# Kernel tuning notes

Hardware: AMD Instinct MI355X
Metric: run time of the kernel (lower is better)

Reference implementation:

```python
import jax, jax.numpy as jnp
import numpy as np

N = 8192
D_IN = 128
D_OUT = 128

def setup_inputs() -> dict:
    key = jax.random.key(0)
    k_x, k_q, k_k, k_v = jax.random.split(key, 4)
    scale = 1.0 / np.sqrt(D_IN)
    return {
        "input": jax.random.normal(k_x, (N, D_IN), dtype=jnp.float32),
        # torch Linear weights: [out_features, in_features]
        "Wq": jax.random.normal(k_q, (D_IN, D_IN), dtype=jnp.float32) * scale,
        "Wk": jax.random.normal(k_k, (D_IN, D_IN), dtype=jnp.float32) * scale,
        "Wv": jax.random.normal(k_v, (D_OUT, D_IN), dtype=jnp.float32) * scale,
    }

def reference(input, Wq, Wk, Wv):
    # torch Linear: y = x @ W.T
    Q = input @ Wq.T          # [N, d_in]
    K = input @ Wk.T          # [N, d_in]
    V = input @ Wv.T          # [N, d_out]
    # NOTE: original module has NO 1/sqrt(d) scaling — keep it faithful.
    W = jax.nn.softmax(Q @ K.T, axis=-1)  # [N, N]
    return W @ V              # [N, d_out]
```

## Files before the change

### kernel.cpp

```cpp
#include <hip/hip_runtime.h>
#include <hip/hip_bf16.h>
#include <stdint.h>

#define N_TOK 8192
#define D 128
#define QTILES (N_TOK / 16)
#define KVB 64
#define KVTILES (N_TOK / KVB)

typedef __attribute__((ext_vector_type(8))) short short8;
typedef __attribute__((ext_vector_type(4))) short short4v;
typedef __attribute__((ext_vector_type(4))) float f32x4;
typedef __attribute__((ext_vector_type(8))) _Float16 half8;
typedef __attribute__((ext_vector_type(4))) _Float16 half4;

__device__ __forceinline__ ushort f2bf(float f) {
    union { float f; uint32_t u; } cv; cv.f = f;
    uint32_t u = cv.u;
    return (ushort)((u + 0x7fffu + ((u >> 16) & 1u)) >> 16);
}
__device__ __forceinline__ float bf2f(ushort h) {
    union { uint32_t u; float f; } cv; cv.u = ((uint32_t)h) << 16;
    return cv.f;
}
__device__ __forceinline__ f32x4 zero4() {
    f32x4 z; z[0] = 0.f; z[1] = 0.f; z[2] = 0.f; z[3] = 0.f; return z;
}

__global__ void cvt_kernel(const float* __restrict__ X, const float* __restrict__ Wq,
                           const float* __restrict__ Wk, const float* __restrict__ Wv,
                           ushort* __restrict__ Xhi, ushort* __restrict__ Xlo,
                           ushort* __restrict__ Whi, ushort* __restrict__ Wlo, int nX) {
    int i = blockIdx.x * blockDim.x + threadIdx.x;
    int e = i * 4;
    int total = nX + 3 * 16384;
    if (e >= total) return;
    const float* src; ushort* dhi; ushort* dlo; int off;
    if (e < nX) { src = X; dhi = Xhi; dlo = Xlo; off = e; }
    else {
        int w = e - nX;
        int m = w >> 14;
        off = w & 16383;
        src = (m == 0) ? Wq : ((m == 1) ? Wk : Wv);
        dhi = Whi + (m << 14);
        dlo = Wlo + (m << 14);
    }
    f32x4 v = *(const f32x4*)(src + off);
    short4v ph, pl;
    #pragma unroll
    for (int r = 0; r < 4; ++r) {
        ushort h = f2bf(v[r]);
        ph[r] = (short)h;
        pl[r] = (short)f2bf(v[r] - bf2f(h));
    }
    *(short4v*)(dhi + off) = ph;
    *(short4v*)(dlo + off) = pl;
}

__global__ __launch_bounds__(256) void proj_kernel(
    const ushort* __restrict__ Xhi, const ushort* __restrict__ Xlo,
    const ushort* __restrict__ Whi, const ushort* __restrict__ Wlo,
    ushort* __restrict__ Qh, ushort* __restrict__ Kh, ushort* __restrict__ Vt) {
    const int tid = threadIdx.x;
    const int lane = tid & 63;
    const int wid = tid >> 6;
    const int g = lane >> 4, r16 = lane & 15;
    const int nbase = blockIdx.x * 16;

    short8 xh[4], xl[4];
    const ushort* xrh = Xhi + (size_t)(nbase + r16) * D + 8 * g;
    const ushort* xrl = Xlo + (size_t)(nbase + r16) * D + 8 * g;
    #pragma unroll
    for (int ds = 0; ds < 4; ++ds) {
        xh[ds] = *(const short8*)(xrh + 32 * ds);
        xl[ds] = *(const short8*)(xrl + 32 * ds);
    }

    #pragma unroll
    for (int m = 0; m < 2; ++m) {
        const ushort* Wh = Whi + m * 16384;
        const ushort* Wl = Wlo + m * 16384;
        ushort* O = m ? Kh : Qh;
        #pragma unroll
        for (int jj = 0; jj < 2; ++jj) {
            int jt = 2 * wid + jj;
            f32x4 acc = zero4();
            const ushort* wrh = Wh + (size_t)(16 * jt + r16) * D + 8 * g;
            const ushort* wrl = Wl + (size_t)(16 * jt + r16) * D + 8 * g;
            #pragma unroll
            for (int ds = 0; ds < 4; ++ds) {
                short8 wh = *(const short8*)(wrh + 32 * ds);
                short8 wl = *(const short8*)(wrl + 32 * ds);
                acc = __builtin_amdgcn_mfma_f32_16x16x32_bf16(wh, xh[ds], acc, 0, 0, 0);
                acc = __builtin_amdgcn_mfma_f32_16x16x32_bf16(wh, xl[ds], acc, 0, 0, 0);
                acc = __builtin_amdgcn_mfma_f32_16x16x32_bf16(wl, xh[ds], acc, 0, 0, 0);
            }
            half4 pk;
            #pragma unroll
            for (int r = 0; r < 4; ++r) pk[r] = (_Float16)acc[r];
            *(half4*)(O + (size_t)(nbase + r16) * D + 16 * jt + 4 * g) = pk;
        }
    }
    {
        const ushort* Wh = Whi + 32768;
        const ushort* Wl = Wlo + 32768;
        #pragma unroll
        for (int jj = 0; jj < 2; ++jj) {
            int jt = 2 * wid + jj;
            f32x4 acc = zero4();
            const ushort* wrh = Wh + (size_t)(16 * jt + r16) * D + 8 * g;
            const ushort* wrl = Wl + (size_t)(16 * jt + r16) * D + 8 * g;
            #pragma unroll
            for (int ds = 0; ds < 4; ++ds) {
                short8 wh = *(const short8*)(wrh + 32 * ds);
                short8 wl = *(const short8*)(wrl + 32 * ds);
                acc = __builtin_amdgcn_mfma_f32_16x16x32_bf16(xh[ds], wh, acc, 0, 0, 0);
                acc = __builtin_amdgcn_mfma_f32_16x16x32_bf16(xl[ds], wh, acc, 0, 0, 0);
                acc = __builtin_amdgcn_mfma_f32_16x16x32_bf16(xh[ds], wl, acc, 0, 0, 0);
            }
            short4v pk;
            #pragma unroll
            for (int r = 0; r < 4; ++r) pk[r] = (short)f2bf(acc[r]);
            *(short4v*)(Vt + (size_t)(16 * jt + r16) * N_TOK + nbase + 4 * g) = pk;
        }
    }
}

template<int NS>
__global__ __launch_bounds__(256, 2) void flash_kernel(
    const ushort* __restrict__ Qh, const ushort* __restrict__ Kh,
    const ushort* __restrict__ Vt, ushort* __restrict__ Opb, float* __restrict__ ML) {
    __shared__ __align__(16) ushort K_lds[2][KVB * D];
    __shared__ __align__(16) ushort V_lds[2][D * KVB];
    __shared__ __align__(16) ushort P_lds[4 * 2048];

    const int tid = threadIdx.x;
    const int lane = tid & 63;
    const int wid = tid >> 6;
    const int g = lane >> 4, r16 = lane & 15;
    const int sp = blockIdx.x % NS;
    const int qg = blockIdx.x / NS;
    const int t0 = (KVTILES * sp) / NS;
    const int t1 = (KVTILES * (sp + 1)) / NS;
    const int qbase = qg * 128 + wid * 32;
    const int pswz = (r16 & 7) << 3;

    half8 qf[2][4];
    #pragma unroll
    for (int qa = 0; qa < 2; ++qa) {
        const ushort* qr = Qh + (size_t)(qbase + 16 * qa + r16) * D + 8 * g;
        #pragma unroll
        for (int ds = 0; ds < 4; ++ds)
            qf[qa][ds] = *(const half8*)(qr + 32 * ds);
    }

    float m[2] = {-INFINITY, -INFINITY}, l[2] = {0.f, 0.f};
    f32x4 o[2][8];
    #pragma unroll
    for (int qa = 0; qa < 2; ++qa)
        #pragma unroll
        for (int dt = 0; dt < 8; ++dt) o[qa][dt] = zero4();

    ushort* P_w = &P_lds[wid * 2048];

    short8 sk[4], sv[4];

    auto LOADT = [&](int it) {
        const int kv = it * KVB;
        #pragma unroll
        for (int rr = 0; rr < 4; ++rr) {
            int idx = tid + 256 * rr;
            int row = idx >> 4, seg = idx & 15;
            sk[rr] = *(const short8*)(Kh + (size_t)(kv + row) * D + seg * 8);
        }
        #pragma unroll
        for (int rr = 0; rr < 4; ++rr) {
            int idx = tid + 256 * rr;
            int row = idx >> 3, seg = idx & 7;
            sv[rr] = *(const short8*)(Vt + (size_t)row * N_TOK + kv + seg * 8);
        }
    };
    auto WRITET = [&](int b) {
        #pragma unroll
        for (int rr = 0; rr < 4; ++rr) {
            int idx = tid + 256 * rr;
            int row = idx >> 4, seg = idx & 15;
            *(short8*)&K_lds[b][(row * 128 + seg * 8) ^ ((row & 7) << 3)] = sk[rr];
        }
        #pragma unroll
        for (int rr = 0; rr < 4; ++rr) {
            int idx = tid + 256 * rr;
            int row = idx >> 3, seg = idx & 7;
            *(short8*)&V_lds[b][(row * 64 + seg * 8) ^ ((row & 7) << 3)] = sv[rr];
        }
    };

    LOADT(t0);
    WRITET(0);
    __syncthreads();

    int buf = 0;
    for (int it = t0; it < t1; ++it) {
        if (it + 1 < t1) LOADT(it + 1);

        const ushort* kb = K_lds[buf];
        const ushort* vb = V_lds[buf];

        f32x4 s[2][4];
        #pragma unroll
        for (int qa = 0; qa < 2; ++qa)
            #pragma unroll
            for (int t = 0; t < 4; ++t) s[qa][t] = zero4();
        __builtin_amdgcn_s_setprio(1);
        #pragma unroll
        for (int t = 0; t < 4; ++t) {
            #pragma unroll
            for (int ds = 0; ds < 4; ++ds) {
                int row = 16 * t + r16;
                half8 kf = *(const half8*)&kb[(row * 128 + 32 * ds + 8 * g) ^ ((row & 7) << 3)];
                #pragma unroll
                for (int qa = 0; qa < 2; ++qa)
                    s[qa][t] = __builtin_amdgcn_mfma_f32_16x16x32_f16(kf, qf[qa][ds], s[qa][t], 0, 0, 0);
            }
        }
        __builtin_amdgcn_s_setprio(0);

        #pragma unroll
        for (int qa = 0; qa < 2; ++qa) {
            float tm = -INFINITY;
            #pragma unroll
            for (int t = 0; t < 4; ++t)
                #pragma unroll
                for (int r = 0; r < 4; ++r) tm = fmaxf(tm, s[qa][t][r]);
            tm = fmaxf(tm, __shfl_xor(tm, 16));
            tm = fmaxf(tm, __shfl_xor(tm, 32));
            float mnew = fmaxf(m[qa], tm);
            float scale = __expf(m[qa] - mnew);
            float psum = 0.f;
            #pragma unroll
            for (int t = 0; t < 4; ++t) {
                short4v pk;
                #pragma unroll
                for (int r = 0; r < 4; ++r) {
                    float p = __expf(s[qa][t][r] - mnew);
                    psum += p;
                    pk[r] = (short)f2bf(p);
                }
                *(short4v*)&P_w[(qa * 1024 + r16 * 64 + 16 * t + 4 * g) ^ pswz] = pk;
            }
            psum += __shfl_xor(psum, 16);
            psum += __shfl_xor(psum, 32);
            l[qa] = l[qa] * scale + psum;
            m[qa] = mnew;
            #pragma unroll
            for (int dt = 0; dt < 8; ++dt) o[qa][dt] *= scale;
        }

        __builtin_amdgcn_s_setprio(1);
        #pragma unroll
        for (int c = 0; c < 2; ++c) {
            short8 pf0 = *(const short8*)&P_w[(r16 * 64 + 32 * c + 8 * g) ^ pswz];
            short8 pf1 = *(const short8*)&P_w[(1024 + r16 * 64 + 32 * c + 8 * g) ^ pswz];
            #pragma unroll
            for (int dt = 0; dt < 8; ++dt) {
                int row = 16 * dt + r16;
                short8 vf = *(const short8*)&vb[(row * 64 + 32 * c + 8 * g) ^ ((row & 7) << 3)];
                o[0][dt] = __builtin_amdgcn_mfma_f32_16x16x32_bf16(vf, pf0, o[0][dt], 0, 0, 0);
                o[1][dt] = __builtin_amdgcn_mfma_f32_16x16x32_bf16(vf, pf1, o[1][dt], 0, 0, 0);
            }
        }
        __builtin_amdgcn_s_setprio(0);

        if (it + 1 < t1) WRITET(buf ^ 1);
        __syncthreads();
        buf ^= 1;
    }

    #pragma unroll
    for (int qa = 0; qa < 2; ++qa) {
        ushort* obase = Opb + ((size_t)sp * N_TOK + qbase + 16 * qa + r16) * D + 4 * g;
        #pragma unroll
        for (int dt = 0; dt < 8; ++dt) {
            short4v pk;
            #pragma unroll
            for (int r = 0; r < 4; ++r) pk[r] = (short)f2bf(o[qa][dt][r]);
            *(short4v*)(obase + 16 * dt) = pk;
        }
        if (g == 0) {
            int qt = (qbase + 16 * qa) >> 4;
            float* ml = ML + ((size_t)sp * QTILES + qt) * 32;
            ml[r16] = m[qa];
            ml[16 + r16] = l[qa];
        }
    }
}

template<int NS>
__global__ void merge_kernel(const ushort* __restrict__ Opb, const float* __restrict__ ML,
                             float* __restrict__ out) {
    int i = blockIdx.x * blockDim.x + threadIdx.x;
    int e = i * 4;
    if (e >= N_TOK * D) return;
    int q = e >> 7;
    int qt = q >> 4, qr = q & 15;
    float mv[NS], lv[NS];
    float M = -INFINITY;
    #pragma unroll
    for (int s = 0; s < NS; ++s) {
        const float* ml = ML + ((size_t)s * QTILES + qt) * 32;
        mv[s] = ml[qr];
        lv[s] = ml[16 + qr];
        M = fmaxf(M, mv[s]);
    }
    float L = 0.f, a[NS];
    #pragma unroll
    for (int s = 0; s < NS; ++s) { a[s] = __expf(mv[s] - M); L += a[s] * lv[s]; }
    float inv = 1.f / L;
    f32x4 acc = zero4();
    #pragma unroll
    for (int s = 0; s < NS; ++s) {
        short4v ov = *(const short4v*)(Opb + (size_t)s * N_TOK * D + e);
        #pragma unroll
        for (int r = 0; r < 4; ++r) acc[r] += bf2f((ushort)ov[r]) * a[s];
    }
    *(f32x4*)(out + e) = acc * inv;
}

extern "C" void kernel_launch(void* const* d_in, const int* in_sizes, int n_in,
                              void* d_out, int out_size, void* d_ws, size_t ws_size,
                              hipStream_t stream) {
    const float* X  = (const float*)d_in[0];
    const float* Wq = (const float*)d_in[1];
    const float* Wk = (const float*)d_in[2];
    const float* Wv = (const float*)d_in[3];
    float* out = (float*)d_out;

    char* ws = (char*)d_ws;
    ushort* Xhi = (ushort*)(ws);
    ushort* Xlo = (ushort*)(ws + 2097152);
    ushort* Whi = (ushort*)(ws + 4194304);
    ushort* Wlo = (ushort*)(ws + 4292608);
    ushort* Qh  = (ushort*)(ws + 4390912);
    ushort* Kh  = (ushort*)(ws + 6488064);
    ushort* Vt  = (ushort*)(ws + 8585216);
    ushort* Opb = (ushort*)(ws + 10682368);

    const size_t op_off = 10682368;
    const size_t need8 = op_off + (size_t)8 * N_TOK * D * 2 + (size_t)8 * QTILES * 32 * 4;

    int nX = N_TOK * D;
    int total4 = (nX + 3 * 16384) / 4;
    cvt_kernel<<<(total4 + 255) / 256, 256, 0, stream>>>(X, Wq, Wk, Wv, Xhi, Xlo, Whi, Wlo, nX);
    proj_kernel<<<QTILES, 256, 0, stream>>>(Xhi, Xlo, Whi, Wlo, Qh, Kh, Vt);

    if (ws_size >= need8) {
        float* ML = (float*)(ws + op_off + (size_t)8 * N_TOK * D * 2);
        flash_kernel<8><<<(N_TOK / 128) * 8, 256, 0, stream>>>(Qh, Kh, Vt, Opb, ML);
        merge_kernel<8><<<(N_TOK * D / 4 + 255) / 256, 256, 0, stream>>>(Opb, ML, out);
    } else {
        float* ML = (float*)(ws + op_off + (size_t)4 * N_TOK * D * 2);
        flash_kernel<4><<<(N_TOK / 128) * 4, 256, 0, stream>>>(Qh, Kh, Vt, Opb, ML);
        merge_kernel<4><<<(N_TOK * D / 4 + 255) / 256, 256, 0, stream>>>(Opb, ML, out);
    }
}
```

Before: 80.91 us.

## Fuse X split into projection, read V directly from global, fp16 P/V path

The hi/lo bf16 split of X moves into the projection kernel, so X no longer makes a separate round trip through global memory. The flash kernel stops staging V through LDS and loads V fragments straight from global memory. It also skips the rescaling of the running max when no lane's max increases, and switches P, V and the partial outputs to fp16 using packed round-toward-zero conversion and the f16 MFMA. These changes cut conversion traffic, LDS footprint and softmax ALU work, but the direct V loads are not double-buffered and fp16 narrows the representable range.

```diff
diff --git a/kernel.cpp b/kernel.cpp
--- a/kernel.cpp
+++ b/kernel.cpp
@@ -13,6 +13,7 @@
 typedef __attribute__((ext_vector_type(4))) float f32x4;
 typedef __attribute__((ext_vector_type(8))) _Float16 half8;
 typedef __attribute__((ext_vector_type(4))) _Float16 half4;
+typedef __attribute__((ext_vector_type(2))) __fp16 fp16x2;
 
 __device__ __forceinline__ ushort f2bf(float f) {
     union { float f; uint32_t u; } cv; cv.f = f;
@@ -27,24 +28,17 @@
     f32x4 z; z[0] = 0.f; z[1] = 0.f; z[2] = 0.f; z[3] = 0.f; return z;
 }
 
-__global__ void cvt_kernel(const float* __restrict__ X, const float* __restrict__ Wq,
-                           const float* __restrict__ Wk, const float* __restrict__ Wv,
-                           ushort* __restrict__ Xhi, ushort* __restrict__ Xlo,
-                           ushort* __restrict__ Whi, ushort* __restrict__ Wlo, int nX) {
+__global__ void cvt_kernel(const float* __restrict__ Wq, const float* __restrict__ Wk,
+                           const float* __restrict__ Wv,
+                           ushort* __restrict__ Whi, ushort* __restrict__ Wlo) {
     int i = blockIdx.x * blockDim.x + threadIdx.x;
-    int e = i * 4;
-    int total = nX + 3 * 16384;
-    if (e >= total) return;
-    const float* src; ushort* dhi; ushort* dlo; int off;
-    if (e < nX) { src = X; dhi = Xhi; dlo = Xlo; off = e; }
-    else {
-        int w = e - nX;
-        int m = w >> 14;
-        off = w & 16383;
-        src = (m == 0) ? Wq : ((m == 1) ? Wk : Wv);
-        dhi = Whi + (m << 14);
-        dlo = Wlo + (m << 14);
-    }
+    int w = i * 4;
+    if (w >= 3 * 16384) return;
+    int m = w >> 14;
+    int off = w & 16383;
+    const float* src = (m == 0) ? Wq : ((m == 1) ? Wk : Wv);
+    ushort* dhi = Whi + (m << 14);
+    ushort* dlo = Wlo + (m << 14);
     f32x4 v = *(const f32x4*)(src + off);
     short4v ph, pl;
     #pragma unroll
@@ -58,7 +52,7 @@
 }
 
 __global__ __launch_bounds__(256) void proj_kernel(
-    const ushort* __restrict__ Xhi, const ushort* __restrict__ Xlo,
+    const float* __restrict__ X,
     const ushort* __restrict__ Whi, const ushort* __restrict__ Wlo,
     ushort* __restrict__ Qh, ushort* __restrict__ Kh, ushort* __restrict__ Vt) {
     const int tid = threadIdx.x;
@@ -68,12 +62,20 @@
     const int nbase = blockIdx.x * 16;
 
     short8 xh[4], xl[4];
-    const ushort* xrh = Xhi + (size_t)(nbase + r16) * D + 8 * g;
-    const ushort* xrl = Xlo + (size_t)(nbase + r16) * D + 8 * g;
+    const float* xr = X + (size_t)(nbase + r16) * D + 8 * g;
     #pragma unroll
     for (int ds = 0; ds < 4; ++ds) {
-        xh[ds] = *(const short8*)(xrh + 32 * ds);
-        xl[ds] = *(const short8*)(xrl + 32 * ds);
+        f32x4 a = *(const f32x4*)(xr + 32 * ds);
+        f32x4 b = *(const f32x4*)(xr + 32 * ds + 4);
+        #pragma unroll
+        for (int j = 0; j < 4; ++j) {
+            ushort h = f2bf(a[j]);
+            xh[ds][j] = (short)h;
+            xl[ds][j] = (short)f2bf(a[j] - bf2f(h));
+            ushort h2 = f2bf(b[j]);
+            xh[ds][4 + j] = (short)h2;
+            xl[ds][4 + j] = (short)f2bf(b[j] - bf2f(h2));
+        }
     }
 
     #pragma unroll
@@ -118,10 +120,10 @@
                 acc = __builtin_amdgcn_mfma_f32_16x16x32_bf16(xl[ds], wh, acc, 0, 0, 0);
                 acc = __builtin_amdgcn_mfma_f32_16x16x32_bf16(xh[ds], wl, acc, 0, 0, 0);
             }
-            short4v pk;
-            #pragma unroll
-            for (int r = 0; r < 4; ++r) pk[r] = (short)f2bf(acc[r]);
-            *(short4v*)(Vt + (size_t)(16 * jt + r16) * N_TOK + nbase + 4 * g) = pk;
+            half4 pk;
+            #pragma unroll
+            for (int r = 0; r < 4; ++r) pk[r] = (_Float16)acc[r];
+            *(half4*)(Vt + (size_t)(16 * jt + r16) * N_TOK + nbase + 4 * g) = pk;
         }
     }
 }
@@ -131,7 +133,6 @@
     const ushort* __restrict__ Qh, const ushort* __restrict__ Kh,
     const ushort* __restrict__ Vt, ushort* __restrict__ Opb, float* __restrict__ ML) {
     __shared__ __align__(16) ushort K_lds[2][KVB * D];
-    __shared__ __align__(16) ushort V_lds[2][D * KVB];
     __shared__ __align__(16) ushort P_lds[4 * 2048];
 
     const int tid = threadIdx.x;
@@ -163,9 +164,9 @@
 
     ushort* P_w = &P_lds[wid * 2048];
 
-    short8 sk[4], sv[4];
-
-    auto LOADT = [&](int it) {
+    short8 sk[4];
+
+    auto LOADK = [&](int it) {
         const int kv = it * KVB;
         #pragma unroll
         for (int rr = 0; rr < 4; ++rr) {
@@ -173,38 +174,26 @@
             int row = idx >> 4, seg = idx & 15;
             sk[rr] = *(const short8*)(Kh + (size_t)(kv + row) * D + seg * 8);
         }
-        #pragma unroll
-        for (int rr = 0; rr < 4; ++rr) {
-            int idx = tid + 256 * rr;
-            int row = idx >> 3, seg = idx & 7;
-            sv[rr] = *(const short8*)(Vt + (size_t)row * N_TOK + kv + seg * 8);
-        }
     };
-    auto WRITET = [&](int b) {
+    auto WRITEK = [&](int b) {
         #pragma unroll
         for (int rr = 0; rr < 4; ++rr) {
             int idx = tid + 256 * rr;
             int row = idx >> 4, seg = idx & 15;
             *(short8*)&K_lds[b][(row * 128 + seg * 8) ^ ((row & 7) << 3)] = sk[rr];
         }
-        #pragma unroll
-        for (int rr = 0; rr < 4; ++rr) {
-            int idx = tid + 256 * rr;
-            int row = idx >> 3, seg = idx & 7;
-            *(short8*)&V_lds[b][(row * 64 + seg * 8) ^ ((row & 7) << 3)] = sv[rr];
-        }
     };
 
-    LOADT(t0);
-    WRITET(0);
+    LOADK(t0);
+    WRITEK(0);
     __syncthreads();
 
     int buf = 0;
     for (int it = t0; it < t1; ++it) {
-        if (it + 1 < t1) LOADT(it + 1);
+        const int kv = it * KVB;
+        if (it + 1 < t1) LOADK(it + 1);
 
         const ushort* kb = K_lds[buf];
-        const ushort* vb = V_lds[buf];
 
         f32x4 s[2][4];
         #pragma unroll
@@ -225,6 +214,15 @@
         }
         __builtin_amdgcn_s_setprio(0);
 
+        half8 vf[2][8];
+        #pragma unroll
+        for (int c = 0; c < 2; ++c)
+            #pragma unroll
+            for (int dt = 0; dt < 8; ++dt) {
+                int row = 16 * dt + r16;
+                vf[c][dt] = *(const half8*)(Vt + (size_t)row * N_TOK + kv + 32 * c + 8 * g);
+            }
+
         #pragma unroll
         for (int qa = 0; qa < 2; ++qa) {
             float tm = -INFINITY;
@@ -234,44 +232,46 @@
                 for (int r = 0; r < 4; ++r) tm = fmaxf(tm, s[qa][t][r]);
             tm = fmaxf(tm, __shfl_xor(tm, 16));
             tm = fmaxf(tm, __shfl_xor(tm, 32));
-            float mnew = fmaxf(m[qa], tm);
-            float scale = __expf(m[qa] - mnew);
+            if (!__all(tm <= m[qa])) {
+                float mnew = fmaxf(m[qa], tm);
+                float scale = __expf(m[qa] - mnew);
+                l[qa] *= scale;
+                #pragma unroll
+                for (int dt = 0; dt < 8; ++dt) o[qa][dt] *= scale;
+                m[qa] = mnew;
+            }
             float psum = 0.f;
             #pragma unroll
             for (int t = 0; t < 4; ++t) {
-                short4v pk;
-                #pragma unroll
-                for (int r = 0; r < 4; ++r) {
-                    float p = __expf(s[qa][t][r] - mnew);
-                    psum += p;
-                    pk[r] = (short)f2bf(p);
-                }
-                *(short4v*)&P_w[(qa * 1024 + r16 * 64 + 16 * t + 4 * g) ^ pswz] = pk;
+                float p0 = __expf(s[qa][t][0] - m[qa]);
+                float p1 = __expf(s[qa][t][1] - m[qa]);
+                float p2 = __expf(s[qa][t][2] - m[qa]);
+                float p3 = __expf(s[qa][t][3] - m[qa]);
+                psum += (p0 + p1) + (p2 + p3);
+                union { fp16x2 h[2]; short4v s4; } u;
+                u.h[0] = __builtin_amdgcn_cvt_pkrtz(p0, p1);
+                u.h[1] = __builtin_amdgcn_cvt_pkrtz(p2, p3);
+                *(short4v*)&P_w[(qa * 1024 + r16 * 64 + 16 * t + 4 * g) ^ pswz] = u.s4;
             }
             psum += __shfl_xor(psum, 16);
             psum += __shfl_xor(psum, 32);
-            l[qa] = l[qa] * scale + psum;
-            m[qa] = mnew;
-            #pragma unroll
-            for (int dt = 0; dt < 8; ++dt) o[qa][dt] *= scale;
+            l[qa] += psum;
         }
 
         __builtin_amdgcn_s_setprio(1);
         #pragma unroll
         for (int c = 0; c < 2; ++c) {
-            short8 pf0 = *(const short8*)&P_w[(r16 * 64 + 32 * c + 8 * g) ^ pswz];
-            short8 pf1 = *(const short8*)&P_w[(1024 + r16 * 64 + 32 * c + 8 * g) ^ pswz];
+            half8 pf0 = *(const half8*)&P_w[(r16 * 64 + 32 * c + 8 * g) ^ pswz];
+            half8 pf1 = *(const half8*)&P_w[(1024 + r16 * 64 + 32 * c + 8 * g) ^ pswz];
             #pragma unroll
             for (int dt = 0; dt < 8; ++dt) {
-                int row = 16 * dt + r16;
-                short8 vf = *(const short8*)&vb[(row * 64 + 32 * c + 8 * g) ^ ((row & 7) << 3)];
-                o[0][dt] = __builtin_amdgcn_mfma_f32_16x16x32_bf16(vf, pf0, o[0][dt], 0, 0, 0);
-                o[1][dt] = __builtin_amdgcn_mfma_f32_16x16x32_bf16(vf, pf1, o[1][dt], 0, 0, 0);
+                o[0][dt] = __builtin_amdgcn_mfma_f32_16x16x32_f16(vf[c][dt], pf0, o[0][dt], 0, 0, 0);
+                o[1][dt] = __builtin_amdgcn_mfma_f32_16x16x32_f16(vf[c][dt], pf1, o[1][dt], 0, 0, 0);
             }
         }
         __builtin_amdgcn_s_setprio(0);
 
-        if (it + 1 < t1) WRITET(buf ^ 1);
+        if (it + 1 < t1) WRITEK(buf ^ 1);
         __syncthreads();
         buf ^= 1;
     }
@@ -281,10 +281,10 @@
         ushort* obase = Opb + ((size_t)sp * N_TOK + qbase + 16 * qa + r16) * D + 4 * g;
         #pragma unroll
         for (int dt = 0; dt < 8; ++dt) {
-            short4v pk;
-            #pragma unroll
-            for (int r = 0; r < 4; ++r) pk[r] = (short)f2bf(o[qa][dt][r]);
-            *(short4v*)(obase + 16 * dt) = pk;
+            half4 pk;
+            #pragma unroll
+            for (int r = 0; r < 4; ++r) pk[r] = (_Float16)o[qa][dt][r];
+            *(half4*)(obase + 16 * dt) = pk;
         }
         if (g == 0) {
             int qt = (qbase + 16 * qa) >> 4;
@@ -319,9 +319,9 @@
     f32x4 acc = zero4();
     #pragma unroll
     for (int s = 0; s < NS; ++s) {
-        short4v ov = *(const short4v*)(Opb + (size_t)s * N_TOK * D + e);
-        #pragma unroll
-        for (int r = 0; r < 4; ++r) acc[r] += bf2f((ushort)ov[r]) * a[s];
+        half4 ov = *(const half4*)(Opb + (size_t)s * N_TOK * D + e);
+        #pragma unroll
+        for (int r = 0; r < 4; ++r) acc[r] += (float)ov[r] * a[s];
     }
     *(f32x4*)(out + e) = acc * inv;
 }
@@ -336,22 +336,18 @@
     float* out = (float*)d_out;
 
     char* ws = (char*)d_ws;
-    ushort* Xhi = (ushort*)(ws);
-    ushort* Xlo = (ushort*)(ws + 2097152);
-    ushort* Whi = (ushort*)(ws + 4194304);
-    ushort* Wlo = (ushort*)(ws + 4292608);
-    ushort* Qh  = (ushort*)(ws + 4390912);
-    ushort* Kh  = (ushort*)(ws + 6488064);
-    ushort* Vt  = (ushort*)(ws + 8585216);
-    ushort* Opb = (ushort*)(ws + 10682368);
-
-    const size_t op_off = 10682368;
+    ushort* Whi = (ushort*)(ws);
+    ushort* Wlo = (ushort*)(ws + 98304);
+    ushort* Qh  = (ushort*)(ws + 196608);
+    ushort* Kh  = (ushort*)(ws + 2293760);
+    ushort* Vt  = (ushort*)(ws + 4390912);
+    ushort* Opb = (ushort*)(ws + 6488064);
+
+    const size_t op_off = 6488064;
     const size_t need8 = op_off + (size_t)8 * N_TOK * D * 2 + (size_t)8 * QTILES * 32 * 4;
 
-    int nX = N_TOK * D;
-    int total4 = (nX + 3 * 16384) / 4;
-    cvt_kernel<<<(total4 + 255) / 256, 256, 0, stream>>>(X, Wq, Wk, Wv, Xhi, Xlo, Whi, Wlo, nX);
-    proj_kernel<<<QTILES, 256, 0, stream>>>(Xhi, Xlo, Whi, Wlo, Qh, Kh, Vt);
+    cvt_kernel<<<48, 256, 0, stream>>>(Wq, Wk, Wv, Whi, Wlo);
+    proj_kernel<<<QTILES, 256, 0, stream>>>(X, Whi, Wlo, Qh, Kh, Vt);
 
     if (ws_size >= need8) {
         float* ML = (float*)(ws + op_off + (size_t)8 * N_TOK * D * 2);
```

After: 116.8 us. 1.44x slower.
